# Kernel tuning notes

Hardware: AMD Instinct MI355X
Metric: run time of the kernel (lower is better)

## Reference

```python
import jax, jax.numpy as jnp
jax.config.update("jax_enable_x64", True)
import numpy as np

BUCKETS = 2147483647  # max int32, as in fused_project call sites
HALF = BUCKETS >> 1
NGRAM_SIZE = 3
# sgnn partition boundaries: indices = [i*(i+1)/2 * P for i in range(n)] + [proj], P=112
IDX = [0, 112, 336, 672]


def _project(sig, mask, seeds):
    """One SgnnProjection partition.

    sig:   [B, M] int64 hash signatures in [0, BUCKETS) (padded ragged rows)
    mask:  [B, M] bool validity of each padded slot (ragged row structure)
    seeds: [H] int64 hash seeds
    returns [B, H] float32
    """
    # value = floormod(abs(sig * seed), buckets); center to [-half, half]
    v = jnp.abs(sig[None, :, :] * seeds[:, None, None]) % BUCKETS  # [H, B, M]
    v = v - jnp.where(v > HALF, BUCKETS, 0)
    vf = v.astype(jnp.float32) * mask[None].astype(jnp.float32)
    counts = jnp.maximum(mask.sum(-1), 1).astype(jnp.float32)  # [B], ragged row lengths
    mean = vf.sum(-1) / counts[None]  # [H, B]  (ragged reduce_mean)
    return (mean / HALF).T  # [B, H]


def setup_inputs() -> dict:
    key = jax.random.key(0)
    k1, k2, k3 = jax.random.split(key, 3)
    signatures = jax.random.randint(k1, (NGRAM_SIZE, 1024, 128), 0, BUCKETS, dtype=jnp.int64)
    mask = jax.random.bernoulli(k2, 0.7, (NGRAM_SIZE, 1024, 128))
    hash_seed = jax.random.randint(k3, (IDX[-1],), 1, BUCKETS, dtype=jnp.int64)
    return {"signatures": signatures, "mask": mask, "hash_seed": hash_seed}


def reference(signatures, mask, hash_seed):
    outs = [
        _project(signatures[i], mask[i], hash_seed[IDX[i]:IDX[i + 1]])
        for i in range(NGRAM_SIZE)
    ]
    return jnp.concatenate(outs, axis=-1).astype(jnp.float32)  # [B, 672]
```

## Files before the change

kernel.cpp:

```cpp
#include <hip/hip_runtime.h>


#define M31    2147483647u
#define HALF_B 1073741823u

__global__ __launch_bounds__(64) void sgnn_prep_kernel(
    const int* __restrict__ sig,
    const int* __restrict__ mask,
    unsigned* __restrict__ msig,
    float* __restrict__ invc,
    unsigned* __restrict__ cnt4)
{
    const int row = blockIdx.x;
    const int t   = threadIdx.x;
    const int g0  = row * 128 + t;
    const int g1  = g0 + 64;
    const int mk0 = mask[g0], mk1 = mask[g1];
    const unsigned v0 = (unsigned)sig[g0], v1 = (unsigned)sig[g1];

    const unsigned long long b0 = __ballot(mk0 != 0);
    const unsigned long long b1 = __ballot(mk1 != 0);
    const unsigned long long lt = (1ULL << t) - 1ULL;
    const int c0   = __popcll(b0);
    const int cnt  = c0 + __popcll(b1);
    const int pos0 = __popcll(b0 & lt);
    const int pos1 = c0 + __popcll(b1 & lt);

    const unsigned base = (unsigned)row * 128u;
    if (mk0) msig[base + pos0] = v0;
    if (mk1) msig[base + pos1] = v1;

    const int c4 = (cnt + 3) & ~3;
    if (cnt + t < c4) msig[base + cnt + t] = 0u;

    if (t == 0) {
        int c = (cnt < 1) ? 1 : cnt;
        invc[row] = 1.0f / ((float)c * 1073741823.0f);
        cnt4[row] = (unsigned)c4;
    }
}

__device__ __forceinline__ void acc_elem(unsigned v, unsigned seed,
                                         unsigned long long& sum, unsigned& q) {
    const unsigned long long p2 =
        (unsigned long long)v * (unsigned long long)seed + (unsigned long long)HALF_B;
    const unsigned lo = (unsigned)p2;
    const unsigned hi = (unsigned)(p2 >> 32);
    const unsigned s  = __builtin_amdgcn_alignbit(hi, lo, 31) + (lo & 0x7FFFFFFFu);
    q   += (s >= M31);
    sum += s;
}

__device__ __forceinline__ void acc4(uint4 a, unsigned seed,
                                     unsigned long long& s0, unsigned long long& s1,
                                     unsigned& q0, unsigned& q1) {
    acc_elem(a.x, seed, s0, q0); acc_elem(a.y, seed, s1, q1);
    acc_elem(a.z, seed, s0, q0); acc_elem(a.w, seed, s1, q1);
}

__global__ __launch_bounds__(256, 8) void sgnn_main_kernel(
    const unsigned* __restrict__ msig,
    const float* __restrict__ invc,
    const unsigned* __restrict__ cnt4,
    const int* __restrict__ seeds,
    float* __restrict__ out,
    int nbatch)
{
    const unsigned t = blockIdx.x * 256u + threadIdx.x;
    const unsigned x = t >> 5;
    const unsigned b = (x * 99865u) >> 21;
    const unsigned h = t - 672u * b;
    const int p = (h < 112u) ? 0 : (h < 336u) ? 1 : 2;

    const unsigned row = (unsigned)(p * nbatch) + b;
    const unsigned* __restrict__ rp = msig + row * 128u;
    const unsigned seed = (unsigned)seeds[h];
    const unsigned n = cnt4[row];

    unsigned long long sum0 = 0, sum1 = 0;
    unsigned q0 = 0, q1 = 0;

    unsigned mm = 0;
    const unsigned n8 = n & ~7u;
    for (; mm < n8; mm += 8) {
        const uint4 a = *(const uint4*)(rp + mm);
        const uint4 c = *(const uint4*)(rp + mm + 4);
        acc4(a, seed, sum0, sum1, q0, q1);
        acc4(c, seed, sum0, sum1, q0, q1);
    }
    if (mm < n) {
        const uint4 a = *(const uint4*)(rp + mm);
        acc4(a, seed, sum0, sum1, q0, q1);
    }

    const long long centered = (long long)(sum0 + sum1)
                             - (long long)(q0 + q1) * 2147483647LL
                             - (long long)n * 1073741823LL;
    out[t] = (float)centered * invc[row];
}

extern "C" void kernel_launch(void* const* d_in, const int* in_sizes, int n_in,
                              void* d_out, int out_size, void* d_ws, size_t ws_size,
                              hipStream_t stream) {
    const int* sig   = (const int*)d_in[0];
    const int* mask  = (const int*)d_in[1];
    const int* seeds = (const int*)d_in[2];
    float* out = (float*)d_out;

    const int nbatch = in_sizes[0] / (3 * 128);
    const int nrows  = 3 * nbatch;
    unsigned* msig = (unsigned*)d_ws;
    float*    invc = (float*)((char*)d_ws + (size_t)nrows * 128 * 4);
    unsigned* c4   = (unsigned*)((char*)d_ws + (size_t)nrows * 132 * 4);

    sgnn_prep_kernel<<<dim3(nrows), dim3(64), 0, stream>>>(sig, mask, msig, invc, c4);
    const int total = nbatch * 672;
    sgnn_main_kernel<<<dim3(total / 256), dim3(256), 0, stream>>>(msig, invc, c4, seeds, out, nbatch);
}
```

Measured before the change: 76.77 us.

## Map waves to uniform partition rows so signature loads become scalar

Reorganizes the main kernel grid so each wavefront handles 64 hash seeds of a single partition row, making the row index wave-uniform via readfirstlane. Signature loads can then be scalar broadcasts instead of per-lane vector loads, cutting vector memory traffic. The inner loop is unrolled to 16 elements and launch bounds are relaxed. In exchange some lanes are idle at partition boundaries (768 lanes for 672 outputs per batch).

```diff
diff --git a/kernel.cpp b/kernel.cpp
--- a/kernel.cpp
+++ b/kernel.cpp
@@ -40,10 +40,11 @@
     }
 }
 
-__device__ __forceinline__ void acc_elem(unsigned v, unsigned seed,
+__device__ __forceinline__ void acc_elem(unsigned sv ,
+                                         unsigned seed ,
                                          unsigned long long& sum, unsigned& q) {
     const unsigned long long p2 =
-        (unsigned long long)v * (unsigned long long)seed + (unsigned long long)HALF_B;
+        (unsigned long long)sv * (unsigned long long)seed + (unsigned long long)HALF_B;
     const unsigned lo = (unsigned)p2;
     const unsigned hi = (unsigned)(p2 >> 32);
     const unsigned s  = __builtin_amdgcn_alignbit(hi, lo, 31) + (lo & 0x7FFFFFFFu);
@@ -51,14 +52,7 @@
     sum += s;
 }
 
-__device__ __forceinline__ void acc4(uint4 a, unsigned seed,
-                                     unsigned long long& s0, unsigned long long& s1,
-                                     unsigned& q0, unsigned& q1) {
-    acc_elem(a.x, seed, s0, q0); acc_elem(a.y, seed, s1, q1);
-    acc_elem(a.z, seed, s0, q0); acc_elem(a.w, seed, s1, q1);
-}
-
-__global__ __launch_bounds__(256, 8) void sgnn_main_kernel(
+__global__ __launch_bounds__(256, 4) void sgnn_main_kernel(
     const unsigned* __restrict__ msig,
     const float* __restrict__ invc,
     const unsigned* __restrict__ cnt4,
@@ -66,37 +60,51 @@
     float* __restrict__ out,
     int nbatch)
 {
-    const unsigned t = blockIdx.x * 256u + threadIdx.x;
-    const unsigned x = t >> 5;
-    const unsigned b = (x * 99865u) >> 21;
-    const unsigned h = t - 672u * b;
-    const int p = (h < 112u) ? 0 : (h < 336u) ? 1 : 2;
+    const unsigned tid  = threadIdx.x;
+    const unsigned lane = tid & 63u;
+    const unsigned W    = blockIdx.x * 4u + (tid >> 6);
+    const unsigned b    = blockIdx.y;
 
-    const unsigned row = (unsigned)(p * nbatch) + b;
-    const unsigned* __restrict__ rp = msig + row * 128u;
-    const unsigned seed = (unsigned)seeds[h];
-    const unsigned n = cnt4[row];
+    unsigned p, h0, hmax;
+    if (W < 2u)      { p = 0; h0 = W * 64u;              hmax = 112u; }
+    else if (W < 6u) { p = 1; h0 = 112u + (W - 2u) * 64u; hmax = 336u; }
+    else             { p = 2; h0 = 336u + (W - 6u) * 64u; hmax = 672u; }
+
+    const unsigned h     = h0 + lane;
+    const bool     valid = (h < hmax);
+    const unsigned h_c   = valid ? h : (hmax - 1u);
+
+    const unsigned row_u = __builtin_amdgcn_readfirstlane(p * (unsigned)nbatch + b);
+    const unsigned* __restrict__ rp = msig + (size_t)row_u * 128u;
+    const unsigned n = cnt4[row_u];
+    const unsigned seed = (unsigned)seeds[h_c];
 
     unsigned long long sum0 = 0, sum1 = 0;
     unsigned q0 = 0, q1 = 0;
 
     unsigned mm = 0;
-    const unsigned n8 = n & ~7u;
-    for (; mm < n8; mm += 8) {
-        const uint4 a = *(const uint4*)(rp + mm);
-        const uint4 c = *(const uint4*)(rp + mm + 4);
-        acc4(a, seed, sum0, sum1, q0, q1);
-        acc4(c, seed, sum0, sum1, q0, q1);
+    const unsigned n16 = n & ~15u;
+    for (; mm < n16; mm += 16) {
+        #pragma unroll
+        for (unsigned jj = 0; jj < 16; jj += 2) {
+            acc_elem(rp[mm + jj],     seed, sum0, q0);
+            acc_elem(rp[mm + jj + 1], seed, sum1, q1);
+        }
     }
-    if (mm < n) {
-        const uint4 a = *(const uint4*)(rp + mm);
-        acc4(a, seed, sum0, sum1, q0, q1);
+    for (; mm < n; mm += 4) {
+        #pragma unroll
+        for (unsigned jj = 0; jj < 4; jj += 2) {
+            acc_elem(rp[mm + jj],     seed, sum0, q0);
+            acc_elem(rp[mm + jj + 1], seed, sum1, q1);
+        }
     }
 
-    const long long centered = (long long)(sum0 + sum1)
-                             - (long long)(q0 + q1) * 2147483647LL
-                             - (long long)n * 1073741823LL;
-    out[t] = (float)centered * invc[row];
+    if (valid) {
+        const long long centered = (long long)(sum0 + sum1)
+                                 - (long long)(q0 + q1) * 2147483647LL
+                                 - (long long)n * 1073741823LL;
+        out[b * 672u + h] = (float)centered * invc[row_u];
+    }
 }
 
 extern "C" void kernel_launch(void* const* d_in, const int* in_sizes, int n_in,
@@ -114,6 +122,5 @@
     unsigned* c4   = (unsigned*)((char*)d_ws + (size_t)nrows * 132 * 4);
 
     sgnn_prep_kernel<<<dim3(nrows), dim3(64), 0, stream>>>(sig, mask, msig, invc, c4);
-    const int total = nbatch * 672;
-    sgnn_main_kernel<<<dim3(total / 256), dim3(256), 0, stream>>>(msig, invc, c4, seeds, out, nbatch);
+    sgnn_main_kernel<<<dim3(3, nbatch), dim3(256), 0, stream>>>(msig, invc, c4, seeds, out, nbatch);
 }
```

Result: no change. 77.33 us (+0.7%).
